# Performance work log

Hardware: AMD Instinct MI355X
Metric: run time of the kernel (lower is better)

## Reference

```python
import jax, jax.numpy as jnp
import numpy as np

N = 100000   # nodes
E = 1600000  # edges (before self-loops)
D = 128      # input_dim
H = 128      # hidden_dim


def setup_inputs() -> dict:
    key = jax.random.key(0)
    ks = jax.random.split(key, 10)
    def lin_w(k, fan_in, fan_out):
        return jax.random.normal(k, (fan_in, fan_out), jnp.float32) / np.float32(np.sqrt(fan_in))
    x = jax.random.normal(ks[0], (N, D), jnp.float32)
    edge_index = jax.random.randint(ks[1], (2, E), 0, N)
    return {
        "x": x,
        "edge_index": edge_index,
        "W0": lin_w(ks[2], D, H), "b0": jnp.zeros((H,), jnp.float32),
        "W1": lin_w(ks[3], H, H), "b1": jnp.zeros((H,), jnp.float32),
        "W2": lin_w(ks[4], H, H), "b2": jnp.zeros((H,), jnp.float32),
        "Wr": lin_w(ks[5], D, H), "br": jnp.zeros((H,), jnp.float32),
    }


def _gcn_norm(edge_index, n):
    # add self-loops, then symmetric normalization D^{-1/2} (A+I) D^{-1/2}
    loop = jnp.arange(n, dtype=edge_index.dtype)
    src = jnp.concatenate([edge_index[0], loop])
    dst = jnp.concatenate([edge_index[1], loop])
    deg = jax.ops.segment_sum(jnp.ones_like(src, dtype=jnp.float32), dst, num_segments=n)
    dinv = jnp.where(deg > 0, jax.lax.rsqrt(deg), 0.0)
    norm = dinv[src] * dinv[dst]  # [E+N]
    return src, dst, norm


def _gcn_layer(x, W, b, src, dst, norm, n):
    h = x @ W                      # [n, H] dense GEMM
    msg = h[src] * norm[:, None]   # gather + scale  [E+N, H]
    out = jax.ops.segment_sum(msg, dst, num_segments=n)  # scatter-add
    return out + b


def reference(x, edge_index, W0, b0, W1, b1, W2, b2, Wr, br):
    n = x.shape[0]
    src, dst, norm = _gcn_norm(edge_index, n)
    residual = x @ Wr + br
    # layer 0: GCN -> relu -> (dropout=identity, eval) -> +residual
    h = jax.nn.relu(_gcn_layer(x, W0, b0, src, dst, norm, n)) + residual
    # layer 1
    h = jax.nn.relu(_gcn_layer(h, W1, b1, src, dst, norm, n))
    # layer 2
    h = jax.nn.relu(_gcn_layer(h, W2, b2, src, dst, norm, n))
    return h
```

## Files before the change

### kernel.cpp

```cpp
#include <hip/hip_runtime.h>
#include <hip/hip_bf16.h>
#include <cstdint>


#define WS_ALIGN(x) (((x) + 255) & ~(size_t)255)

typedef __bf16 bf16x8 __attribute__((ext_vector_type(8)));
typedef float  floatx4 __attribute__((ext_vector_type(4)));

static __device__ __forceinline__ float bf_lo(unsigned u) {
  return __builtin_bit_cast(float, u << 16);
}
static __device__ __forceinline__ float bf_hi(unsigned u) {
  return __builtin_bit_cast(float, u & 0xffff0000u);
}
static __device__ __forceinline__ unsigned short f2bs(float f) {
  unsigned u = __builtin_bit_cast(unsigned, f);
  return (unsigned short)((u + 0x7fffu + ((u >> 16) & 1u)) >> 16);
}
static __device__ __forceinline__ unsigned pack2(float a, float b) {
  return (unsigned)f2bs(a) | ((unsigned)f2bs(b) << 16);
}

__global__ void k_cntprep(const int* __restrict__ dstv, int E, int eb,
                          int* __restrict__ cnt, int* __restrict__ pos,
                          const float* __restrict__ x, unsigned* __restrict__ xb,
                          int n4, int xbn,
                          const float* __restrict__ W0, const float* __restrict__ W1,
                          const float* __restrict__ W2, const float* __restrict__ Wr,
                          unsigned short* __restrict__ Wt) {
  int g = blockIdx.x;
  int vc = g / 3, rem = g % 3;
  if (rem == 0) {
    if (vc < eb) {
      int e = vc * 256 + threadIdx.x;
      if (e < E) pos[e] = atomicAdd(&cnt[dstv[e]], 1);
    }
  } else {
    int p = 2 * vc + rem - 1;
    if (p < xbn) {
      int i = p * 256 + threadIdx.x;
      if (i < n4) {
        float4 v = ((const float4*)x)[i];
        uint2 o;
        o.x = pack2(v.x, v.y);
        o.y = pack2(v.z, v.w);
        ((uint2*)xb)[i] = o;
      }
    } else if (p < xbn + 256) {
      int wv = p - xbn;
      int mat = wv >> 6, blk = wv & 63;
      const float* W = mat == 0 ? W0 : mat == 1 ? W1 : mat == 2 ? W2 : Wr;
      unsigned short* T = Wt + (size_t)mat * 16384;
      int i = blk * 256 + threadIdx.x;
      int k = i >> 7, nn = i & 127;
      T[nn * 128 + k] = f2bs(W[i]);
    }
  }
}

__global__ void k_scat(const int* __restrict__ srcv, const int* __restrict__ dstv,
                       const int* __restrict__ pos, int E, int nb,
                       const int* __restrict__ cnt, float* __restrict__ dinv,
                       int* __restrict__ epk, int2* __restrict__ ovf,
                       int* __restrict__ ovfn, int n) {
  int b = blockIdx.x;
  if (b < nb) {
    int i = b * 256 + threadIdx.x;
    if (i < n) {
      int c = cnt[i];
      dinv[i] = rsqrtf((float)(c + 1));
      int cm = c < 32 ? c : 32;
      int cp = (cm + 7) & ~7;
      for (int k = cm; k < cp; k++) epk[(size_t)i * 32 + k] = n;
    }
  } else {
    int e = (b - nb) * 256 + threadIdx.x;
    if (e < E) {
      int s = srcv[e], d = dstv[e];
      int r = pos[e];
      if (r < 32) {
        epk[(size_t)d * 32 + r] = s;
      } else {
        int o = atomicAdd(ovfn, 1);
        if (o < E) {
          int2 t; t.x = s; t.y = d;
          ovf[o] = t;
        }
      }
    }
  }
}

static __device__ __forceinline__ void gemm_tile(
    int vt, const unsigned short* __restrict__ Xb,
    const unsigned short* sWt,
    const float* __restrict__ bias, const float* __restrict__ dv,
    unsigned short* __restrict__ Y, int n) {
  const int lane = threadIdx.x & 63;
  const int wave = threadIdx.x >> 6;
  const int l15 = lane & 15;
  const int quad = lane >> 4;
  const int rbase = vt * 64 + wave * 16;

  const bf16x8* sW8 = (const bf16x8*)sWt;
  bf16x8 b[8][4];
#pragma unroll
  for (int ct = 0; ct < 8; ct++)
#pragma unroll
    for (int kc = 0; kc < 4; kc++)
      b[ct][kc] = sW8[(ct * 16 + l15) * 16 + kc * 4 + quad];

  int row = rbase + l15;
  row = row < n ? row : n - 1;
  const bf16x8* X8 = (const bf16x8*)Xb;
  bf16x8 a[4];
#pragma unroll
  for (int kc = 0; kc < 4; kc++)
    a[kc] = X8[(size_t)row * 16 + kc * 4 + quad];

  floatx4 acc[8];
#pragma unroll
  for (int ct = 0; ct < 8; ct++) acc[ct] = (floatx4){0.f, 0.f, 0.f, 0.f};

#pragma unroll
  for (int kc = 0; kc < 4; kc++)
#pragma unroll
    for (int ct = 0; ct < 8; ct++)
      acc[ct] = __builtin_amdgcn_mfma_f32_16x16x32_bf16(a[kc], b[ct][kc], acc[ct], 0, 0, 0);

  const int orow = rbase + quad * 4;
  float4 dvv;
  dvv.x = 1.f; dvv.y = 1.f; dvv.z = 1.f; dvv.w = 1.f;
  if (dv) {
    int od = orow < n ? orow : 0;
    dvv = *(const float4*)(dv + od);
  }
#pragma unroll
  for (int ct = 0; ct < 8; ct++) {
    const int c = ct * 16 + l15;
    const float bv = bias ? bias[c] : 0.f;
#pragma unroll
    for (int r4 = 0; r4 < 4; r4++) {
      int r = orow + r4;
      float dm = r4 == 0 ? dvv.x : r4 == 1 ? dvv.y : r4 == 2 ? dvv.z : dvv.w;
      if (r < n) Y[(size_t)r * 128 + c] = f2bs(acc[ct][r4] * dm + bv);
    }
  }
}

static __device__ __forceinline__ void stage_w(const unsigned short* Wm,
                                               unsigned short* sWt) {
  const uint4* s4 = (const uint4*)Wm;
  uint4* d4 = (uint4*)sWt;
  for (int i = threadIdx.x; i < 2048; i += 256) d4[i] = s4[i];
  __syncthreads();
}

__global__ __launch_bounds__(256, 2) void k_gemm_mfma(
    const unsigned short* __restrict__ Xb,
    const unsigned short* __restrict__ Wt,
    const float* __restrict__ bias,
    const float* __restrict__ dv,
    unsigned short* __restrict__ Y,
    int n) {
  __shared__ unsigned short sWt[128 * 128];
  stage_w(Wt, sWt);
  gemm_tile(blockIdx.x, Xb, sWt, bias, dv, Y, n);
}

__global__ __launch_bounds__(256, 2) void k_gemmRA(
    const unsigned short* __restrict__ xb,
    const unsigned short* __restrict__ Wtr, const float* __restrict__ brs,
    unsigned short* __restrict__ R,
    const unsigned short* __restrict__ Wt0, const float* __restrict__ dinv,
    unsigned short* __restrict__ A,
    int gb, int n) {
  __shared__ unsigned short sWt[128 * 128];
  if ((int)blockIdx.x < gb) {
    stage_w(Wtr, sWt);
    gemm_tile(blockIdx.x, xb, sWt, brs, nullptr, R, n);
  } else {
    stage_w(Wt0, sWt);
    gemm_tile(blockIdx.x - gb, xb, sWt, nullptr, dinv, A, n);
  }
}

static __device__ __forceinline__ void add8(uint4 h, float* a) {
  a[0] += bf_lo(h.x); a[1] += bf_hi(h.x);
  a[2] += bf_lo(h.y); a[3] += bf_hi(h.y);
  a[4] += bf_lo(h.z); a[5] += bf_hi(h.z);
  a[6] += bf_lo(h.w); a[7] += bf_hi(h.w);
}

__global__ __launch_bounds__(256, 4) void k_agg(
    const uint4* __restrict__ H,
    const int* __restrict__ cnt,
    const int* __restrict__ epk,
    const float* __restrict__ dinv,
    const float* __restrict__ bias,
    const uint4* __restrict__ resid,
    uint4* __restrict__ outb,
    float4* __restrict__ outf,
    const int2* __restrict__ ovf, const int* __restrict__ ovfn,
    int n, int Ecap) {
  int node = blockIdx.x * 16 + (threadIdx.x >> 4);
  int l = threadIdx.x & 15;
  if (node >= n) return;

  int tot = cnt[node];
  int cm = tot < 32 ? tot : 32;
  int pdeg = (cm + 7) & ~7;

  uint4 hv = H[(size_t)node * 16 + l];
  float a[8];
  a[0] = bf_lo(hv.x); a[1] = bf_hi(hv.x);
  a[2] = bf_lo(hv.y); a[3] = bf_hi(hv.y);
  a[4] = bf_lo(hv.z); a[5] = bf_hi(hv.z);
  a[6] = bf_lo(hv.w); a[7] = bf_hi(hv.w);

  const int4* epk4 = (const int4*)(epk + (size_t)node * 32);
  for (int j = 0; j < pdeg; j += 8) {
    int4 e0 = epk4[j >> 2];
    int4 e1 = epk4[(j >> 2) + 1];
    uint4 h0 = H[(size_t)(unsigned)e0.x * 16 + l];
    uint4 h1 = H[(size_t)(unsigned)e0.y * 16 + l];
    uint4 h2 = H[(size_t)(unsigned)e0.z * 16 + l];
    uint4 h3 = H[(size_t)(unsigned)e0.w * 16 + l];
    uint4 h4 = H[(size_t)(unsigned)e1.x * 16 + l];
    uint4 h5 = H[(size_t)(unsigned)e1.y * 16 + l];
    uint4 h6 = H[(size_t)(unsigned)e1.z * 16 + l];
    uint4 h7 = H[(size_t)(unsigned)e1.w * 16 + l];
    add8(h0, a); add8(h1, a); add8(h2, a); add8(h3, a);
    add8(h4, a); add8(h5, a); add8(h6, a); add8(h7, a);
  }
  if (tot > 32) {
    int no = *ovfn;
    no = no < Ecap ? no : Ecap;
    for (int i = 0; i < no; i++) {
      int2 t = ovf[i];
      if (t.y == node) add8(H[(size_t)(unsigned)t.x * 16 + l], a);
    }
  }

  float dn = dinv[node];
  float4 bl = ((const float4*)bias)[l * 2];
  float4 bh = ((const float4*)bias)[l * 2 + 1];
  a[0] = fmaxf(fmaf(a[0], dn, bl.x), 0.f); a[1] = fmaxf(fmaf(a[1], dn, bl.y), 0.f);
  a[2] = fmaxf(fmaf(a[2], dn, bl.z), 0.f); a[3] = fmaxf(fmaf(a[3], dn, bl.w), 0.f);
  a[4] = fmaxf(fmaf(a[4], dn, bh.x), 0.f); a[5] = fmaxf(fmaf(a[5], dn, bh.y), 0.f);
  a[6] = fmaxf(fmaf(a[6], dn, bh.z), 0.f); a[7] = fmaxf(fmaf(a[7], dn, bh.w), 0.f);
  if (resid) {
    uint4 r = resid[(size_t)node * 16 + l];
    a[0] += bf_lo(r.x); a[1] += bf_hi(r.x);
    a[2] += bf_lo(r.y); a[3] += bf_hi(r.y);
    a[4] += bf_lo(r.z); a[5] += bf_hi(r.z);
    a[6] += bf_lo(r.w); a[7] += bf_hi(r.w);
  }
  if (outb) {
    uint4 o;
    o.x = pack2(a[0], a[1]); o.y = pack2(a[2], a[3]);
    o.z = pack2(a[4], a[5]); o.w = pack2(a[6], a[7]);
    outb[(size_t)node * 16 + l] = o;
  } else {
    float4 o0; o0.x = a[0]; o0.y = a[1]; o0.z = a[2]; o0.w = a[3];
    float4 o1; o1.x = a[4]; o1.y = a[5]; o1.z = a[6]; o1.w = a[7];
    outf[(size_t)node * 32 + l * 2] = o0;
    outf[(size_t)node * 32 + l * 2 + 1] = o1;
  }
}

extern "C" void kernel_launch(void* const* d_in, const int* in_sizes, int n_in,
                              void* d_out, int out_size, void* d_ws, size_t ws_size,
                              hipStream_t stream) {
  const float* x  = (const float*)d_in[0];
  const int* edges = (const int*)d_in[1];
  const float* W0 = (const float*)d_in[2];
  const float* b0 = (const float*)d_in[3];
  const float* W1 = (const float*)d_in[4];
  const float* b1 = (const float*)d_in[5];
  const float* W2 = (const float*)d_in[6];
  const float* b2 = (const float*)d_in[7];
  const float* Wr = (const float*)d_in[8];
  const float* br = (const float*)d_in[9];

  int N = in_sizes[0] / 128;
  int E = in_sizes[1] / 2;
  const int* src = edges;
  const int* dst = edges + E;

  char* ws = (char*)d_ws;
  size_t off = 0;
  auto alloc = [&](size_t bytes) -> void* {
    void* p = ws + off; off = WS_ALIGN(off + bytes); return p;
  };
  int*   cnt  = (int*)  alloc((size_t)N * 4);
  int*   ovfn = (int*)  alloc(256);
  float* dinv = (float*)alloc((size_t)N * 4);
  int2*  ovf  = (int2*) alloc((size_t)E * 8);
  int*   epk  = (int*)  alloc((size_t)N * 32 * 4);
  unsigned short* xb = (unsigned short*)alloc((size_t)N * 128 * 2);
  unsigned short* Wt = (unsigned short*)alloc((size_t)4 * 16384 * 2);
  unsigned short* A  = (unsigned short*)alloc(((size_t)N + 1) * 128 * 2);
  unsigned short* Hb = (unsigned short*)alloc((size_t)N * 128 * 2);
  unsigned short* R  = (unsigned short*)alloc((size_t)N * 128 * 2);
  int* pos = (int*)A;
  (void)ws_size; (void)n_in; (void)out_size;

  int n4 = N * 128 / 4;
  int eb = (E + 255) / 256;
  int xbn = (n4 + 255) / 256;
  int nb = (N + 255) / 256;
  int gb = (N + 63) / 64;
  int ab = (N + 15) / 16;
  unsigned short* Wt0 = Wt;
  unsigned short* Wt1 = Wt + 16384;
  unsigned short* Wt2 = Wt + 2 * 16384;
  unsigned short* Wtr = Wt + 3 * 16384;

  hipMemsetAsync(cnt, 0, (size_t)((char*)ovfn - (char*)cnt) + 4, stream);
  hipMemsetAsync(A + (size_t)N * 128, 0, 256, stream);

  int pb = xbn + 256;
  int pbh = (pb + 1) / 2;
  int T3 = 3 * (eb > pbh ? eb : pbh);
  k_cntprep<<<T3, 256, 0, stream>>>(dst, E, eb, cnt, pos,
                                    x, (unsigned*)xb, n4, xbn,
                                    W0, W1, W2, Wr, Wt);
  k_scat<<<nb + eb, 256, 0, stream>>>(src, dst, pos, E, nb, cnt, dinv,
                                      epk, ovf, ovfn, N);
  k_gemmRA<<<2 * gb, 256, 0, stream>>>(xb, Wtr, br, R, Wt0, dinv, A, gb, N);

  k_agg<<<ab, 256, 0, stream>>>((const uint4*)A, cnt, epk, dinv, b0,
                                (const uint4*)R, (uint4*)Hb, nullptr, ovf, ovfn, N, E);
  k_gemm_mfma<<<gb, 256, 0, stream>>>(Hb, Wt1, nullptr, dinv, A, N);
  k_agg<<<ab, 256, 0, stream>>>((const uint4*)A, cnt, epk, dinv, b1,
                                nullptr, (uint4*)R, nullptr, ovf, ovfn, N, E);
  k_gemm_mfma<<<gb, 256, 0, stream>>>(R, Wt2, nullptr, dinv, A, N);
  k_agg<<<ab, 256, 0, stream>>>((const uint4*)A, cnt, epk, dinv, b2,
                                nullptr, nullptr, (float4*)d_out, ovf, ovfn, N, E);
}
```

Measured before the change: 472.6 us.

## Fuse residual GEMM into the count/prep kernel, reading fp32 x directly

The residual projection x@Wr+br moves out of the combined residual/layer-0 GEMM kernel and into the first prep kernel as a fourth block role. Those blocks read fp32 x, convert it to bf16 in registers, and transpose Wr into LDS themselves. The aim is to overlap the residual GEMM with the edge-counting atomics and the x conversion, leaving the later GEMM launch to do only the layer-0 product. The cost is that every prep block now reserves 32 KB of LDS under a 2-blocks-per-SIMD launch bound, which may lower occupancy of the atomic and convert blocks. Each GEMM block also repeats a strided fp32 transpose of Wr.

```diff
diff --git a/kernel.cpp b/kernel.cpp
--- a/kernel.cpp
+++ b/kernel.cpp
@@ -22,21 +22,143 @@
   return (unsigned)f2bs(a) | ((unsigned)f2bs(b) << 16);
 }
 
-__global__ void k_cntprep(const int* __restrict__ dstv, int E, int eb,
-                          int* __restrict__ cnt, int* __restrict__ pos,
-                          const float* __restrict__ x, unsigned* __restrict__ xb,
-                          int n4, int xbn,
-                          const float* __restrict__ W0, const float* __restrict__ W1,
-                          const float* __restrict__ W2, const float* __restrict__ Wr,
-                          unsigned short* __restrict__ Wt) {
+static __device__ __forceinline__ void gemm_tile(
+    int vt, const unsigned short* __restrict__ Xb,
+    const unsigned short* sWt,
+    const float* __restrict__ bias, const float* __restrict__ dv,
+    unsigned short* __restrict__ Y, int n) {
+  const int lane = threadIdx.x & 63;
+  const int wave = threadIdx.x >> 6;
+  const int l15 = lane & 15;
+  const int quad = lane >> 4;
+  const int rbase = vt * 64 + wave * 16;
+
+  const bf16x8* sW8 = (const bf16x8*)sWt;
+  bf16x8 b[8][4];
+#pragma unroll
+  for (int ct = 0; ct < 8; ct++)
+#pragma unroll
+    for (int kc = 0; kc < 4; kc++)
+      b[ct][kc] = sW8[(ct * 16 + l15) * 16 + kc * 4 + quad];
+
+  int row = rbase + l15;
+  row = row < n ? row : n - 1;
+  const bf16x8* X8 = (const bf16x8*)Xb;
+  bf16x8 a[4];
+#pragma unroll
+  for (int kc = 0; kc < 4; kc++)
+    a[kc] = X8[(size_t)row * 16 + kc * 4 + quad];
+
+  floatx4 acc[8];
+#pragma unroll
+  for (int ct = 0; ct < 8; ct++) acc[ct] = (floatx4){0.f, 0.f, 0.f, 0.f};
+
+#pragma unroll
+  for (int kc = 0; kc < 4; kc++)
+#pragma unroll
+    for (int ct = 0; ct < 8; ct++)
+      acc[ct] = __builtin_amdgcn_mfma_f32_16x16x32_bf16(a[kc], b[ct][kc], acc[ct], 0, 0, 0);
+
+  const int orow = rbase + quad * 4;
+  float4 dvv;
+  dvv.x = 1.f; dvv.y = 1.f; dvv.z = 1.f; dvv.w = 1.f;
+  if (dv) {
+    int od = orow < n ? orow : 0;
+    dvv = *(const float4*)(dv + od);
+  }
+#pragma unroll
+  for (int ct = 0; ct < 8; ct++) {
+    const int c = ct * 16 + l15;
+    const float bv = bias ? bias[c] : 0.f;
+#pragma unroll
+    for (int r4 = 0; r4 < 4; r4++) {
+      int r = orow + r4;
+      float dm = r4 == 0 ? dvv.x : r4 == 1 ? dvv.y : r4 == 2 ? dvv.z : dvv.w;
+      if (r < n) Y[(size_t)r * 128 + c] = f2bs(acc[ct][r4] * dm + bv);
+    }
+  }
+}
+
+static __device__ __forceinline__ void gemm_tile_f32x(
+    int vt, const float* __restrict__ Xf, const unsigned short* sWt,
+    const float* __restrict__ bias, unsigned short* __restrict__ Y, int n) {
+  const int lane = threadIdx.x & 63;
+  const int wave = threadIdx.x >> 6;
+  const int l15 = lane & 15;
+  const int quad = lane >> 4;
+  const int rbase = vt * 64 + wave * 16;
+
+  const bf16x8* sW8 = (const bf16x8*)sWt;
+  bf16x8 b[8][4];
+#pragma unroll
+  for (int ct = 0; ct < 8; ct++)
+#pragma unroll
+    for (int kc = 0; kc < 4; kc++)
+      b[ct][kc] = sW8[(ct * 16 + l15) * 16 + kc * 4 + quad];
+
+  int row = rbase + l15;
+  row = row < n ? row : n - 1;
+  const float4* X4 = (const float4*)Xf;
+  bf16x8 a[4];
+#pragma unroll
+  for (int kc = 0; kc < 4; kc++) {
+    float4 f0 = X4[(size_t)row * 32 + (kc * 4 + quad) * 2];
+    float4 f1 = X4[(size_t)row * 32 + (kc * 4 + quad) * 2 + 1];
+    uint4 u;
+    u.x = pack2(f0.x, f0.y); u.y = pack2(f0.z, f0.w);
+    u.z = pack2(f1.x, f1.y); u.w = pack2(f1.z, f1.w);
+    a[kc] = __builtin_bit_cast(bf16x8, u);
+  }
+
+  floatx4 acc[8];
+#pragma unroll
+  for (int ct = 0; ct < 8; ct++) acc[ct] = (floatx4){0.f, 0.f, 0.f, 0.f};
+
+#pragma unroll
+  for (int kc = 0; kc < 4; kc++)
+#pragma unroll
+    for (int ct = 0; ct < 8; ct++)
+      acc[ct] = __builtin_amdgcn_mfma_f32_16x16x32_bf16(a[kc], b[ct][kc], acc[ct], 0, 0, 0);
+
+  const int orow = rbase + quad * 4;
+#pragma unroll
+  for (int ct = 0; ct < 8; ct++) {
+    const int c = ct * 16 + l15;
+    const float bv = bias[c];
+#pragma unroll
+    for (int r4 = 0; r4 < 4; r4++) {
+      int r = orow + r4;
+      if (r < n) Y[(size_t)r * 128 + c] = f2bs(acc[ct][r4] + bv);
+    }
+  }
+}
+
+static __device__ __forceinline__ void stage_w(const unsigned short* Wm,
+                                               unsigned short* sWt) {
+  const uint4* s4 = (const uint4*)Wm;
+  uint4* d4 = (uint4*)sWt;
+  for (int i = threadIdx.x; i < 2048; i += 256) d4[i] = s4[i];
+  __syncthreads();
+}
+
+__global__ __launch_bounds__(256, 2) void k_cntprep(
+    const int* __restrict__ dstv, int E, int eb,
+    int* __restrict__ cnt, int* __restrict__ pos,
+    const float* __restrict__ x, unsigned* __restrict__ xb,
+    int n4, int xbn,
+    const float* __restrict__ W0, const float* __restrict__ W1,
+    const float* __restrict__ W2, unsigned short* __restrict__ Wt,
+    const float* __restrict__ Wr, const float* __restrict__ brs,
+    unsigned short* __restrict__ R, int gb, int n) {
+  __shared__ unsigned short sWt[128 * 128];
   int g = blockIdx.x;
-  int vc = g / 3, rem = g % 3;
+  int vc = g >> 2, rem = g & 3;
   if (rem == 0) {
     if (vc < eb) {
       int e = vc * 256 + threadIdx.x;
       if (e < E) pos[e] = atomicAdd(&cnt[dstv[e]], 1);
     }
-  } else {
+  } else if (rem < 3) {
     int p = 2 * vc + rem - 1;
     if (p < xbn) {
       int i = p * 256 + threadIdx.x;
@@ -47,14 +169,23 @@
         o.y = pack2(v.z, v.w);
         ((uint2*)xb)[i] = o;
       }
-    } else if (p < xbn + 256) {
+    } else if (p < xbn + 192) {
       int wv = p - xbn;
       int mat = wv >> 6, blk = wv & 63;
-      const float* W = mat == 0 ? W0 : mat == 1 ? W1 : mat == 2 ? W2 : Wr;
+      const float* W = mat == 0 ? W0 : mat == 1 ? W1 : W2;
       unsigned short* T = Wt + (size_t)mat * 16384;
       int i = blk * 256 + threadIdx.x;
       int k = i >> 7, nn = i & 127;
       T[nn * 128 + k] = f2bs(W[i]);
+    }
+  } else {
+    if (vc < gb) {
+      for (int j = (int)threadIdx.x; j < 16384; j += 256) {
+        int nn = j >> 7, k = j & 127;
+        sWt[j] = f2bs(Wr[k * 128 + nn]);
+      }
+      __syncthreads();
+      gemm_tile_f32x(vc, x, sWt, brs, R, n);
     }
   }
 }
@@ -92,71 +223,6 @@
   }
 }
 
-static __device__ __forceinline__ void gemm_tile(
-    int vt, const unsigned short* __restrict__ Xb,
-    const unsigned short* sWt,
-    const float* __restrict__ bias, const float* __restrict__ dv,
-    unsigned short* __restrict__ Y, int n) {
-  const int lane = threadIdx.x & 63;
-  const int wave = threadIdx.x >> 6;
-  const int l15 = lane & 15;
-  const int quad = lane >> 4;
-  const int rbase = vt * 64 + wave * 16;
-
-  const bf16x8* sW8 = (const bf16x8*)sWt;
-  bf16x8 b[8][4];
-#pragma unroll
-  for (int ct = 0; ct < 8; ct++)
-#pragma unroll
-    for (int kc = 0; kc < 4; kc++)
-      b[ct][kc] = sW8[(ct * 16 + l15) * 16 + kc * 4 + quad];
-
-  int row = rbase + l15;
-  row = row < n ? row : n - 1;
-  const bf16x8* X8 = (const bf16x8*)Xb;
-  bf16x8 a[4];
-#pragma unroll
-  for (int kc = 0; kc < 4; kc++)
-    a[kc] = X8[(size_t)row * 16 + kc * 4 + quad];
-
-  floatx4 acc[8];
-#pragma unroll
-  for (int ct = 0; ct < 8; ct++) acc[ct] = (floatx4){0.f, 0.f, 0.f, 0.f};
-
-#pragma unroll
-  for (int kc = 0; kc < 4; kc++)
-#pragma unroll
-    for (int ct = 0; ct < 8; ct++)
-      acc[ct] = __builtin_amdgcn_mfma_f32_16x16x32_bf16(a[kc], b[ct][kc], acc[ct], 0, 0, 0);
-
-  const int orow = rbase + quad * 4;
-  float4 dvv;
-  dvv.x = 1.f; dvv.y = 1.f; dvv.z = 1.f; dvv.w = 1.f;
-  if (dv) {
-    int od = orow < n ? orow : 0;
-    dvv = *(const float4*)(dv + od);
-  }
-#pragma unroll
-  for (int ct = 0; ct < 8; ct++) {
-    const int c = ct * 16 + l15;
-    const float bv = bias ? bias[c] : 0.f;
-#pragma unroll
-    for (int r4 = 0; r4 < 4; r4++) {
-      int r = orow + r4;
-      float dm = r4 == 0 ? dvv.x : r4 == 1 ? dvv.y : r4 == 2 ? dvv.z : dvv.w;
-      if (r < n) Y[(size_t)r * 128 + c] = f2bs(acc[ct][r4] * dm + bv);
-    }
-  }
-}
-
-static __device__ __forceinline__ void stage_w(const unsigned short* Wm,
-                                               unsigned short* sWt) {
-  const uint4* s4 = (const uint4*)Wm;
-  uint4* d4 = (uint4*)sWt;
-  for (int i = threadIdx.x; i < 2048; i += 256) d4[i] = s4[i];
-  __syncthreads();
-}
-
 __global__ __launch_bounds__(256, 2) void k_gemm_mfma(
     const unsigned short* __restrict__ Xb,
     const unsigned short* __restrict__ Wt,
@@ -167,23 +233,6 @@
   __shared__ unsigned short sWt[128 * 128];
   stage_w(Wt, sWt);
   gemm_tile(blockIdx.x, Xb, sWt, bias, dv, Y, n);
-}
-
-__global__ __launch_bounds__(256, 2) void k_gemmRA(
-    const unsigned short* __restrict__ xb,
-    const unsigned short* __restrict__ Wtr, const float* __restrict__ brs,
-    unsigned short* __restrict__ R,
-    const unsigned short* __restrict__ Wt0, const float* __restrict__ dinv,
-    unsigned short* __restrict__ A,
-    int gb, int n) {
-  __shared__ unsigned short sWt[128 * 128];
-  if ((int)blockIdx.x < gb) {
-    stage_w(Wtr, sWt);
-    gemm_tile(blockIdx.x, xb, sWt, brs, nullptr, R, n);
-  } else {
-    stage_w(Wt0, sWt);
-    gemm_tile(blockIdx.x - gb, xb, sWt, nullptr, dinv, A, n);
-  }
 }
 
 static __device__ __forceinline__ void add8(uint4 h, float* a) {
@@ -316,20 +365,20 @@
   unsigned short* Wt0 = Wt;
   unsigned short* Wt1 = Wt + 16384;
   unsigned short* Wt2 = Wt + 2 * 16384;
-  unsigned short* Wtr = Wt + 3 * 16384;
 
   hipMemsetAsync(cnt, 0, (size_t)((char*)ovfn - (char*)cnt) + 4, stream);
   hipMemsetAsync(A + (size_t)N * 128, 0, 256, stream);
 
-  int pb = xbn + 256;
+  int pb = xbn + 192;
   int pbh = (pb + 1) / 2;
-  int T3 = 3 * (eb > pbh ? eb : pbh);
-  k_cntprep<<<T3, 256, 0, stream>>>(dst, E, eb, cnt, pos,
-                                    x, (unsigned*)xb, n4, xbn,
-                                    W0, W1, W2, Wr, Wt);
+  int m4 = eb > pbh ? eb : pbh;
+  m4 = m4 > gb ? m4 : gb;
+  k_cntprep<<<4 * m4, 256, 0, stream>>>(dst, E, eb, cnt, pos,
+                                        x, (unsigned*)xb, n4, xbn,
+                                        W0, W1, W2, Wt, Wr, br, R, gb, N);
   k_scat<<<nb + eb, 256, 0, stream>>>(src, dst, pos, E, nb, cnt, dinv,
                                       epk, ovf, ovfn, N);
-  k_gemmRA<<<2 * gb, 256, 0, stream>>>(xb, Wtr, br, R, Wt0, dinv, A, gb, N);
+  k_gemm_mfma<<<gb, 256, 0, stream>>>(xb, Wt0, nullptr, dinv, A, N);
 
   k_agg<<<ab, 256, 0, stream>>>((const uint4*)A, cnt, epk, dinv, b0,
                                 (const uint4*)R, (uint4*)Hb, nullptr, ovf, ovfn, N, E);
```

Measured after the change: 611.1 us. +29.3%, slower.
